# Performance work log

Measured on AMD Instinct MI355X. Metric: run time of the kernel, lower is better.

Reference implementation:

```python
import jax, jax.numpy as jnp
import numpy as np

N_NODES = 50000
N_EDGES = 800000
D_N = 64      # node feature dim
D_E = 64      # edge feature dim
HID = 128     # MLP hidden dim
D_OUT = 64    # edge/node MLP output dim


def _mlp_params(key, d_in, d_hid, d_out):
    k1, k2 = jax.random.split(key)
    s1 = 1.0 / np.sqrt(d_in)
    s2 = 1.0 / np.sqrt(d_hid)
    return (
        jax.random.uniform(k1, (d_in, d_hid), jnp.float32, -s1, s1),
        jnp.zeros((d_hid,), jnp.float32),
        jax.random.uniform(k2, (d_hid, d_out), jnp.float32, -s2, s2),
        jnp.zeros((d_out,), jnp.float32),
    )


def setup_inputs() -> dict:
    key = jax.random.key(0)
    ks = jax.random.split(key, 7)
    nf = jax.random.normal(ks[0], (N_NODES, D_N), jnp.float32)
    ef = jax.random.normal(ks[1], (N_EDGES, D_E), jnp.float32)
    src = jax.random.randint(ks[2], (N_EDGES,), 0, N_NODES, jnp.int64)
    dst = jax.random.randint(ks[3], (N_EDGES,), 0, N_NODES, jnp.int64)
    We1, be1, We2, be2 = _mlp_params(ks[4], 2 * D_N + D_E, HID, D_OUT)
    Wa1, ba1, Wa2, ba2 = _mlp_params(ks[5], 2 * D_N + D_E, HID, D_OUT)
    Wn1, bn1, Wn2, bn2 = _mlp_params(ks[6], D_OUT + D_N, HID, D_OUT)
    return dict(nf=nf, ef=ef, src=src, dst=dst,
                We1=We1, be1=be1, We2=We2, be2=be2,
                Wa1=Wa1, ba1=ba1, Wa2=Wa2, ba2=ba2,
                Wn1=Wn1, bn1=bn1, Wn2=Wn2, bn2=bn2)


def _mlp(x, W1, b1, W2, b2):
    return jax.nn.relu(x @ W1 + b1) @ W2 + b2


def reference(nf, ef, src, dst,
              We1, be1, We2, be2,
              Wa1, ba1, Wa2, ba2,
              Wn1, bn1, Wn2, bn2):
    # edge update: gather src/dst node feats, concat with edge feats  [E, 2*D_N + D_E]
    x_e = jnp.concatenate([nf[src], nf[dst], ef], axis=-1)
    e_out = _mlp(x_e, We1, be1, We2, be2)                 # [E, D_OUT]
    gate = jax.nn.sigmoid(_mlp(x_e, Wa1, ba1, Wa2, ba2))  # [E, D_OUT]
    updated_ef = gate * e_out                              # message m == updated edge feat
    # scatter-sum messages into destination nodes
    agg_m = jax.ops.segment_sum(updated_ef, dst, num_segments=N_NODES)  # [N, D_OUT]
    # node update
    x_n = jnp.concatenate([agg_m, nf], axis=-1)            # [N, D_OUT + D_N]
    updated_nf = _mlp(x_n, Wn1, bn1, Wn2, bn2)             # [N, D_OUT]
    return updated_nf, updated_ef
```

## Files before the change

### kernel.cpp

```cpp
#include <hip/hip_runtime.h>

#define NN 50000
#define NE 800000
#define NB 196

typedef float f32x4 __attribute__((ext_vector_type(4)));
typedef short s16x8 __attribute__((ext_vector_type(8)));
typedef unsigned short u16;

__device__ __forceinline__ u16 f2bf(float f) {
  union { float f; unsigned u; } v; v.f = f;
  unsigned r = v.u + 0x7FFFu + ((v.u >> 16) & 1u);
  return (u16)(r >> 16);
}

__device__ __forceinline__ void st_bf4(u16* p, f32x4 v) {
  ushort4 pv;
  pv.x = f2bf(v.x); pv.y = f2bf(v.y); pv.z = f2bf(v.z); pv.w = f2bf(v.w);
  *(ushort4*)p = pv;
}

__device__ __forceinline__ void pack_one(const float* __restrict__ W, int N,
                                         u16* __restrict__ out, int t) {
  int j = t & 7, lane = (t >> 3) & 63, f = t >> 9;
  int NT = N >> 4;
  int nt = f % NT, ks = f / NT;
  int row = ks * 32 + ((lane >> 4) << 3) + j;
  int col = nt * 16 + (lane & 15);
  out[t] = f2bf(W[row * N + col]);
}

__global__ void pack_kernel(const float* __restrict__ We1, const float* __restrict__ We2,
                            const float* __restrict__ Wa1, const float* __restrict__ Wa2,
                            const float* __restrict__ Wn1, const float* __restrict__ Wn2,
                            u16* __restrict__ out) {
  int t = blockIdx.x * 256 + threadIdx.x;
  if (t < 24576)      pack_one(We1, 128, out,          t);
  else if (t < 32768) pack_one(We2, 64,  out + 24576,  t - 24576);
  else if (t < 57344) pack_one(Wa1, 128, out + 32768,  t - 32768);
  else if (t < 65536) pack_one(Wa2, 64,  out + 57344,  t - 57344);
  else if (t < 81920) pack_one(Wn1, 128, out + 65536,  t - 65536);
  else if (t < 90112) pack_one(Wn2, 64,  out + 81920,  t - 81920);
}


__global__ void count_kernel(const int* __restrict__ dst, int* __restrict__ cnt) {
  int e = blockIdx.x * 256 + threadIdx.x;
  if (e < NE) atomicAdd(cnt + dst[e], 1);
}

__global__ __launch_bounds__(256)
void scan1_kernel(const int* __restrict__ cnt, int* __restrict__ part,
                  int* __restrict__ bsum) {
  int b = blockIdx.x, t = threadIdx.x;
  int i = b * 256 + t;
  int v = (i < NN) ? cnt[i] : 0;
  int lane = t & 63, wv = t >> 6;
  int s = v;
  #pragma unroll
  for (int d = 1; d < 64; d <<= 1) {
    int u = __shfl_up(s, d, 64);
    if (lane >= d) s += u;
  }
  __shared__ int ws[4];
  if (lane == 63) ws[wv] = s;
  __syncthreads();
  int add = 0;
  #pragma unroll
  for (int k = 0; k < 3; ++k) if (k < wv) add += ws[k];
  s += add;
  if (i < NN) part[i] = s - v;
  if (t == 255) bsum[b] = s;
}

__global__ __launch_bounds__(256)
void scan2_kernel(const int* __restrict__ bsum, int* __restrict__ bbase,
                  int* __restrict__ off) {
  int t = threadIdx.x;
  int v = (t < NB) ? bsum[t] : 0;
  int lane = t & 63, wv = t >> 6;
  int s = v;
  #pragma unroll
  for (int d = 1; d < 64; d <<= 1) {
    int u = __shfl_up(s, d, 64);
    if (lane >= d) s += u;
  }
  __shared__ int ws[4];
  if (lane == 63) ws[wv] = s;
  __syncthreads();
  int add = 0;
  #pragma unroll
  for (int k = 0; k < 3; ++k) if (k < wv) add += ws[k];
  s += add;
  if (t < NB) bbase[t] = s - v;
  if (t == NB - 1) off[NN] = s;
}

__global__ __launch_bounds__(256)
void scan3_kernel(const int* __restrict__ part, const int* __restrict__ bbase,
                  int* __restrict__ off, int* __restrict__ cursor) {
  int b = blockIdx.x, t = threadIdx.x;
  int i = b * 256 + t;
  if (i < NN) {
    int o = part[i] + bbase[b];
    off[i] = o;
    cursor[i] = o;
  }
}

__global__ void fill_kernel(const int* __restrict__ src, const int* __restrict__ dst,
                            int* __restrict__ cursor, int4* __restrict__ tup) {
  int e = blockIdx.x * 256 + threadIdx.x;
  if (e < NE) {
    int d = dst[e];
    int slot = atomicAdd(cursor + d, 1);
    int4 t4; t4.x = src[e]; t4.y = d; t4.z = e; t4.w = 0;
    tup[slot] = t4;
  }
}


__device__ __forceinline__ void edge_mlps(
    u16* xe , u16* hs , int lane,
    const u16* __restrict__ W1e, const float* __restrict__ b1e, const u16* __restrict__ W2e,
    const u16* __restrict__ W1a, const float* __restrict__ b1a, const u16* __restrict__ W2a,
    f32x4 eo[4], f32x4 go[4]) {
  const int m = lane & 15, q = lane >> 4;
  s16x8 a1[6];
  #pragma unroll
  for (int k = 0; k < 6; ++k)
    a1[k] = *(const s16x8*)(xe + m * 200 + k * 32 + q * 8);

  f32x4 acc[8];
  #pragma unroll
  for (int i = 0; i < 8; ++i) { acc[i][0] = 0.f; acc[i][1] = 0.f; acc[i][2] = 0.f; acc[i][3] = 0.f; }
  #pragma unroll
  for (int nt = 0; nt < 8; ++nt)
    #pragma unroll
    for (int k = 0; k < 6; ++k) {
      s16x8 b = *(const s16x8*)(W1e + ((size_t)(k * 8 + nt) * 64 + lane) * 8);
      acc[nt] = __builtin_amdgcn_mfma_f32_16x16x32_bf16(a1[k], b, acc[nt], 0, 0, 0);
    }
  #pragma unroll
  for (int nt = 0; nt < 8; ++nt) {
    float bv = b1e[nt * 16 + m];
    #pragma unroll
    for (int r = 0; r < 4; ++r) {
      float h = acc[nt][r] + bv;
      h = h > 0.f ? h : 0.f;
      hs[(q * 4 + r) * 136 + nt * 16 + m] = f2bf(h);
    }
  }
  __syncthreads();

  s16x8 a2[4];
  #pragma unroll
  for (int k = 0; k < 4; ++k)
    a2[k] = *(const s16x8*)(hs + m * 136 + k * 32 + q * 8);
  #pragma unroll
  for (int i = 0; i < 4; ++i) { eo[i][0] = 0.f; eo[i][1] = 0.f; eo[i][2] = 0.f; eo[i][3] = 0.f; }
  #pragma unroll
  for (int nt = 0; nt < 4; ++nt)
    #pragma unroll
    for (int k = 0; k < 4; ++k) {
      s16x8 b = *(const s16x8*)(W2e + ((size_t)(k * 4 + nt) * 64 + lane) * 8);
      eo[nt] = __builtin_amdgcn_mfma_f32_16x16x32_bf16(a2[k], b, eo[nt], 0, 0, 0);
    }

  f32x4 accg[8];
  #pragma unroll
  for (int i = 0; i < 8; ++i) { accg[i][0] = 0.f; accg[i][1] = 0.f; accg[i][2] = 0.f; accg[i][3] = 0.f; }
  #pragma unroll
  for (int nt = 0; nt < 8; ++nt)
    #pragma unroll
    for (int k = 0; k < 6; ++k) {
      s16x8 b = *(const s16x8*)(W1a + ((size_t)(k * 8 + nt) * 64 + lane) * 8);
      accg[nt] = __builtin_amdgcn_mfma_f32_16x16x32_bf16(a1[k], b, accg[nt], 0, 0, 0);
    }
  __syncthreads();
  #pragma unroll
  for (int nt = 0; nt < 8; ++nt) {
    float bv = b1a[nt * 16 + m];
    #pragma unroll
    for (int r = 0; r < 4; ++r) {
      float h = accg[nt][r] + bv;
      h = h > 0.f ? h : 0.f;
      hs[(q * 4 + r) * 136 + nt * 16 + m] = f2bf(h);
    }
  }
  __syncthreads();

  s16x8 a2g[4];
  #pragma unroll
  for (int k = 0; k < 4; ++k)
    a2g[k] = *(const s16x8*)(hs + m * 136 + k * 32 + q * 8);
  #pragma unroll
  for (int i = 0; i < 4; ++i) { go[i][0] = 0.f; go[i][1] = 0.f; go[i][2] = 0.f; go[i][3] = 0.f; }
  #pragma unroll
  for (int nt = 0; nt < 4; ++nt)
    #pragma unroll
    for (int k = 0; k < 4; ++k) {
      s16x8 b = *(const s16x8*)(W2a + ((size_t)(k * 4 + nt) * 64 + lane) * 8);
      go[nt] = __builtin_amdgcn_mfma_f32_16x16x32_bf16(a2g[k], b, go[nt], 0, 0, 0);
    }
}

__device__ __forceinline__ void node_mlp(
    u16* xn , u16* hn , int lane,
    const u16* __restrict__ W1n, const float* __restrict__ b1n, const u16* __restrict__ W2n,
    f32x4 o[4]) {
  const int m = lane & 15, q = lane >> 4;
  s16x8 a1[4];
  #pragma unroll
  for (int k = 0; k < 4; ++k)
    a1[k] = *(const s16x8*)(xn + m * 136 + k * 32 + q * 8);
  f32x4 acc[8];
  #pragma unroll
  for (int i = 0; i < 8; ++i) { acc[i][0] = 0.f; acc[i][1] = 0.f; acc[i][2] = 0.f; acc[i][3] = 0.f; }
  #pragma unroll
  for (int nt = 0; nt < 8; ++nt)
    #pragma unroll
    for (int k = 0; k < 4; ++k) {
      s16x8 b = *(const s16x8*)(W1n + ((size_t)(k * 8 + nt) * 64 + lane) * 8);
      acc[nt] = __builtin_amdgcn_mfma_f32_16x16x32_bf16(a1[k], b, acc[nt], 0, 0, 0);
    }
  #pragma unroll
  for (int nt = 0; nt < 8; ++nt) {
    float bv = b1n[nt * 16 + m];
    #pragma unroll
    for (int r = 0; r < 4; ++r) {
      float h = acc[nt][r] + bv;
      h = h > 0.f ? h : 0.f;
      hn[(q * 4 + r) * 136 + nt * 16 + m] = f2bf(h);
    }
  }
  __syncthreads();
  s16x8 a2[4];
  #pragma unroll
  for (int k = 0; k < 4; ++k)
    a2[k] = *(const s16x8*)(hn + m * 136 + k * 32 + q * 8);
  #pragma unroll
  for (int i = 0; i < 4; ++i) { o[i][0] = 0.f; o[i][1] = 0.f; o[i][2] = 0.f; o[i][3] = 0.f; }
  #pragma unroll
  for (int nt = 0; nt < 4; ++nt)
    #pragma unroll
    for (int k = 0; k < 4; ++k) {
      s16x8 b = *(const s16x8*)(W2n + ((size_t)(k * 4 + nt) * 64 + lane) * 8);
      o[nt] = __builtin_amdgcn_mfma_f32_16x16x32_bf16(a2[k], b, o[nt], 0, 0, 0);
    }
}


__global__ __launch_bounds__(256, 3)
void edge_sorted(const float* __restrict__ nf, const float* __restrict__ ef,
                 const int4* __restrict__ tup,
                 const u16* __restrict__ W1e, const float* __restrict__ b1e,
                 const u16* __restrict__ W2e, const float* __restrict__ b2e,
                 const u16* __restrict__ W1a, const float* __restrict__ b1a,
                 const u16* __restrict__ W2a, const float* __restrict__ b2a,
                 float* __restrict__ out_ef, float* __restrict__ msg) {
  __shared__ u16 xe[4][16 * 200];
  __shared__ u16 hs[4][16 * 136];
  __shared__ int se[4][16];
  const int w = threadIdx.x >> 6, lane = threadIdx.x & 63;
  const int e0 = blockIdx.x * 64 + w * 16;
  const int er = lane >> 4, c4 = (lane & 15) * 4;

  #pragma unroll
  for (int g = 0; g < 4; ++g) {
    int el = g * 4 + er;
    int slot = e0 + el;
    int4 t4 = tup[slot];
    if (c4 == 0) se[w][el] = t4.z;
    f32x4 fs = *(const f32x4*)(nf + (size_t)t4.x * 64 + c4);
    f32x4 fd = *(const f32x4*)(nf + (size_t)t4.y * 64 + c4);
    f32x4 fe = *(const f32x4*)(ef + (size_t)t4.z * 64 + c4);
    u16* row = &xe[w][el * 200];
    st_bf4(row + c4, fs);
    st_bf4(row + 64 + c4, fd);
    st_bf4(row + 128 + c4, fe);
  }
  __syncthreads();

  f32x4 eo[4], go[4];
  edge_mlps(xe[w], hs[w], lane, W1e, b1e, W2e, W1a, b1a, W2a, eo, go);

  const int m = lane & 15, q = lane >> 4;
  #pragma unroll
  for (int nt = 0; nt < 4; ++nt) {
    int col = nt * 16 + m;
    float be2v = b2e[col], ba2v = b2a[col];
    #pragma unroll
    for (int r = 0; r < 4; ++r) {
      int rowi = q * 4 + r;
      float ev = eo[nt][r] + be2v;
      float gv = go[nt][r] + ba2v;
      float gs = 1.f / (1.f + __expf(-gv));
      float val = gs * ev;
      out_ef[(size_t)se[w][rowi] * 64 + col] = val;
      msg[(size_t)(e0 + rowi) * 64 + col] = val;
    }
  }
}


__global__ __launch_bounds__(256, 3)
void edge_atomic(const float* __restrict__ nf, const float* __restrict__ ef,
                 const int* __restrict__ src, const int* __restrict__ dst,
                 const u16* __restrict__ W1e, const float* __restrict__ b1e,
                 const u16* __restrict__ W2e, const float* __restrict__ b2e,
                 const u16* __restrict__ W1a, const float* __restrict__ b1a,
                 const u16* __restrict__ W2a, const float* __restrict__ b2a,
                 float* __restrict__ out_ef, float* __restrict__ agg) {
  __shared__ u16 xe[4][16 * 200];
  __shared__ u16 hs[4][16 * 136];
  __shared__ int sdst[4][16];
  const int w = threadIdx.x >> 6, lane = threadIdx.x & 63;
  const int e0 = blockIdx.x * 64 + w * 16;
  const int er = lane >> 4, c4 = (lane & 15) * 4;

  #pragma unroll
  for (int g = 0; g < 4; ++g) {
    int el = g * 4 + er;
    int e = e0 + el;
    int s = src[e], d = dst[e];
    if (c4 == 0) sdst[w][el] = d;
    f32x4 fs = *(const f32x4*)(nf + (size_t)s * 64 + c4);
    f32x4 fd = *(const f32x4*)(nf + (size_t)d * 64 + c4);
    f32x4 fe = *(const f32x4*)(ef + (size_t)e * 64 + c4);
    u16* row = &xe[w][el * 200];
    st_bf4(row + c4, fs);
    st_bf4(row + 64 + c4, fd);
    st_bf4(row + 128 + c4, fe);
  }
  __syncthreads();

  f32x4 eo[4], go[4];
  edge_mlps(xe[w], hs[w], lane, W1e, b1e, W2e, W1a, b1a, W2a, eo, go);

  const int m = lane & 15, q = lane >> 4;
  #pragma unroll
  for (int nt = 0; nt < 4; ++nt) {
    int col = nt * 16 + m;
    float be2v = b2e[col], ba2v = b2a[col];
    #pragma unroll
    for (int r = 0; r < 4; ++r) {
      int rowi = q * 4 + r;
      float ev = eo[nt][r] + be2v;
      float gv = go[nt][r] + ba2v;
      float gs = 1.f / (1.f + __expf(-gv));
      float val = gs * ev;
      out_ef[(size_t)(e0 + rowi) * 64 + col] = val;
      atomicAdd(agg + (size_t)sdst[w][rowi] * 64 + col, val);
    }
  }
}


__global__ __launch_bounds__(256, 4)
void node_sorted(const float* __restrict__ nf, const float* __restrict__ msg,
                 const int* __restrict__ off,
                 const u16* __restrict__ W1n, const float* __restrict__ b1n,
                 const u16* __restrict__ W2n, const float* __restrict__ b2n,
                 float* __restrict__ out_nf) {
  __shared__ u16 xn[4][16 * 136];
  __shared__ u16 hn[4][16 * 136];
  const int w = threadIdx.x >> 6, lane = threadIdx.x & 63;
  const int n0 = blockIdx.x * 64 + w * 16;
  const int er = lane >> 4, c4 = (lane & 15) * 4;

  #pragma unroll
  for (int g = 0; g < 4; ++g) {
    int nl = g * 4 + er;
    int n = n0 + nl; if (n >= NN) n = NN - 1;
    f32x4 fn4 = *(const f32x4*)(nf + (size_t)n * 64 + c4);
    int beg = off[n], end = off[n + 1];
    f32x4 s0, s1, s2, s3;
    s0[0]=0.f;s0[1]=0.f;s0[2]=0.f;s0[3]=0.f; s1=s0; s2=s0; s3=s0;
    int i = beg;
    for (; i + 4 <= end; i += 4) {
      f32x4 m0 = *(const f32x4*)(msg + (size_t)(i    ) * 64 + c4);
      f32x4 m1 = *(const f32x4*)(msg + (size_t)(i + 1) * 64 + c4);
      f32x4 m2 = *(const f32x4*)(msg + (size_t)(i + 2) * 64 + c4);
      f32x4 m3 = *(const f32x4*)(msg + (size_t)(i + 3) * 64 + c4);
      s0 += m0; s1 += m1; s2 += m2; s3 += m3;
    }
    for (; i < end; ++i)
      s0 += *(const f32x4*)(msg + (size_t)i * 64 + c4);
    f32x4 s = (s0 + s1) + (s2 + s3);
    u16* row = &xn[w][nl * 136];
    st_bf4(row + c4, s);
    st_bf4(row + 64 + c4, fn4);
  }
  __syncthreads();

  f32x4 o[4];
  node_mlp(xn[w], hn[w], lane, W1n, b1n, W2n, o);

  const int m = lane & 15, q = lane >> 4;
  #pragma unroll
  for (int nt = 0; nt < 4; ++nt) {
    int col = nt * 16 + m;
    float bv = b2n[col];
    #pragma unroll
    for (int r = 0; r < 4; ++r) {
      int n = n0 + q * 4 + r;
      if (n < NN) out_nf[(size_t)n * 64 + col] = o[nt][r] + bv;
    }
  }
}


__global__ __launch_bounds__(256, 4)
void node_direct(const float* __restrict__ nf, const float* __restrict__ agg,
                 const u16* __restrict__ W1n, const float* __restrict__ b1n,
                 const u16* __restrict__ W2n, const float* __restrict__ b2n,
                 float* __restrict__ out_nf) {
  __shared__ u16 xn[4][16 * 136];
  __shared__ u16 hn[4][16 * 136];
  const int w = threadIdx.x >> 6, lane = threadIdx.x & 63;
  const int n0 = blockIdx.x * 64 + w * 16;
  const int er = lane >> 4, c4 = (lane & 15) * 4;

  #pragma unroll
  for (int g = 0; g < 4; ++g) {
    int nl = g * 4 + er;
    int n = n0 + nl; if (n >= NN) n = NN - 1;
    f32x4 fa = *(const f32x4*)(agg + (size_t)n * 64 + c4);
    f32x4 fn4 = *(const f32x4*)(nf + (size_t)n * 64 + c4);
    u16* row = &xn[w][nl * 136];
    st_bf4(row + c4, fa);
    st_bf4(row + 64 + c4, fn4);
  }
  __syncthreads();

  f32x4 o[4];
  node_mlp(xn[w], hn[w], lane, W1n, b1n, W2n, o);

  const int m = lane & 15, q = lane >> 4;
  #pragma unroll
  for (int nt = 0; nt < 4; ++nt) {
    int col = nt * 16 + m;
    float bv = b2n[col];
    #pragma unroll
    for (int r = 0; r < 4; ++r) {
      int n = n0 + q * 4 + r;
      if (n < NN) out_nf[(size_t)n * 64 + col] = o[nt][r] + bv;
    }
  }
}

extern "C" void kernel_launch(void* const* d_in, const int* in_sizes, int n_in,
                              void* d_out, int out_size, void* d_ws, size_t ws_size,
                              hipStream_t stream) {
  const float* nf  = (const float*)d_in[0];
  const float* ef  = (const float*)d_in[1];
  const int*   src = (const int*)d_in[2];
  const int*   dst = (const int*)d_in[3];
  const float* We1 = (const float*)d_in[4];
  const float* be1 = (const float*)d_in[5];
  const float* We2 = (const float*)d_in[6];
  const float* be2 = (const float*)d_in[7];
  const float* Wa1 = (const float*)d_in[8];
  const float* ba1 = (const float*)d_in[9];
  const float* Wa2 = (const float*)d_in[10];
  const float* ba2 = (const float*)d_in[11];
  const float* Wn1 = (const float*)d_in[12];
  const float* bn1 = (const float*)d_in[13];
  const float* Wn2 = (const float*)d_in[14];
  const float* bn2 = (const float*)d_in[15];
  float* out = (float*)d_out;
  float* out_ef = out + (size_t)NN * 64;

  char* ws = (char*)d_ws;
  u16* pk = (u16*)ws;

  const size_t CNT_OFF  = 180224;
  const size_t PART_OFF = 380224;
  const size_t OFF_OFF  = 580224;
  const size_t CUR_OFF  = 780240;
  const size_t BSUM_OFF = 980240;
  const size_t BBAS_OFF = 981024;
  const size_t TUP_OFF  = 981824;
  const size_t MSG_OFF  = 13781824;
  const size_t NEED     = MSG_OFF + (size_t)NE * 64 * 4;

  pack_kernel<<<352, 256, 0, stream>>>(We1, We2, Wa1, Wa2, Wn1, Wn2, pk);

  if (ws_size >= NEED) {
    int*  cnt    = (int*)(ws + CNT_OFF);
    int*  part   = (int*)(ws + PART_OFF);
    int*  off    = (int*)(ws + OFF_OFF);
    int*  cursor = (int*)(ws + CUR_OFF);
    int*  bsum   = (int*)(ws + BSUM_OFF);
    int*  bbase  = (int*)(ws + BBAS_OFF);
    int4* tup    = (int4*)(ws + TUP_OFF);
    float* msg   = (float*)(ws + MSG_OFF);

    hipMemsetAsync(cnt, 0, (size_t)NN * sizeof(int), stream);
    count_kernel<<<(NE + 255) / 256, 256, 0, stream>>>(dst, cnt);
    scan1_kernel<<<NB, 256, 0, stream>>>(cnt, part, bsum);
    scan2_kernel<<<1, 256, 0, stream>>>(bsum, bbase, off);
    scan3_kernel<<<NB, 256, 0, stream>>>(part, bbase, off, cursor);
    fill_kernel<<<(NE + 255) / 256, 256, 0, stream>>>(src, dst, cursor, tup);
    edge_sorted<<<NE / 64, 256, 0, stream>>>(nf, ef, tup,
        pk, be1, pk + 24576, be2, pk + 32768, ba1, pk + 57344, ba2,
        out_ef, msg);
    node_sorted<<<(NN + 63) / 64, 256, 0, stream>>>(nf, msg, off,
        pk + 65536, bn1, pk + 81920, bn2, out);
  } else {
    float* agg = (float*)(ws + CNT_OFF);
    hipMemsetAsync(agg, 0, (size_t)NN * 64 * sizeof(float), stream);
    edge_atomic<<<NE / 64, 256, 0, stream>>>(nf, ef, src, dst,
        pk, be1, pk + 24576, be2, pk + 32768, ba1, pk + 57344, ba2,
        out_ef, agg);
    node_direct<<<(NN + 63) / 64, 256, 0, stream>>>(nf, agg,
        pk + 65536, bn1, pk + 81920, bn2, out);
  }
}
```

Baseline: 805.3 us.

## Replace sorted message buffer with segmented atomic aggregation and XCD-aware block remap

The edge kernel no longer writes a full per-edge message buffer for a later segmented reduction. It now pre-reduces consecutive same-destination rows within each 16-edge tile, using wave shuffles when the whole tile shares one destination, and atomically adds the partial sums into a zeroed node aggregate that node_direct consumes. This removes about 200 MB of message writes and reads plus the offset array, at the cost of float atomics to global memory and a memset. Block indices are also remapped so contiguous sorted edge chunks land on the same XCD, which should improve L2 locality for the atomics.

```diff
diff --git a/kernel.cpp b/kernel.cpp
--- a/kernel.cpp
+++ b/kernel.cpp
@@ -74,8 +74,7 @@
 }
 
 __global__ __launch_bounds__(256)
-void scan2_kernel(const int* __restrict__ bsum, int* __restrict__ bbase,
-                  int* __restrict__ off) {
+void scan2_kernel(const int* __restrict__ bsum, int* __restrict__ bbase) {
   int t = threadIdx.x;
   int v = (t < NB) ? bsum[t] : 0;
   int lane = t & 63, wv = t >> 6;
@@ -93,19 +92,14 @@
   for (int k = 0; k < 3; ++k) if (k < wv) add += ws[k];
   s += add;
   if (t < NB) bbase[t] = s - v;
-  if (t == NB - 1) off[NN] = s;
 }
 
 __global__ __launch_bounds__(256)
 void scan3_kernel(const int* __restrict__ part, const int* __restrict__ bbase,
-                  int* __restrict__ off, int* __restrict__ cursor) {
+                  int* __restrict__ cursor) {
   int b = blockIdx.x, t = threadIdx.x;
   int i = b * 256 + t;
-  if (i < NN) {
-    int o = part[i] + bbase[b];
-    off[i] = o;
-    cursor[i] = o;
-  }
+  if (i < NN) cursor[i] = part[i] + bbase[b];
 }
 
 __global__ void fill_kernel(const int* __restrict__ src, const int* __restrict__ dst,
@@ -258,12 +252,17 @@
                  const u16* __restrict__ W2e, const float* __restrict__ b2e,
                  const u16* __restrict__ W1a, const float* __restrict__ b1a,
                  const u16* __restrict__ W2a, const float* __restrict__ b2a,
-                 float* __restrict__ out_ef, float* __restrict__ msg) {
+                 float* __restrict__ out_ef, float* __restrict__ agg) {
   __shared__ u16 xe[4][16 * 200];
   __shared__ u16 hs[4][16 * 136];
   __shared__ int se[4][16];
+  __shared__ int sdst[4][16];
   const int w = threadIdx.x >> 6, lane = threadIdx.x & 63;
-  const int e0 = blockIdx.x * 64 + w * 16;
+  const int nwg = gridDim.x;
+  const int qq = nwg >> 3, rr = nwg & 7;
+  const int xcd = blockIdx.x & 7, idx = blockIdx.x >> 3;
+  const int bid = (xcd < rr ? xcd * (qq + 1) : rr * (qq + 1) + (xcd - rr) * qq) + idx;
+  const int e0 = bid * 64 + w * 16;
   const int er = lane >> 4, c4 = (lane & 15) * 4;
 
   #pragma unroll
@@ -271,7 +270,7 @@
     int el = g * 4 + er;
     int slot = e0 + el;
     int4 t4 = tup[slot];
-    if (c4 == 0) se[w][el] = t4.z;
+    if (c4 == 0) { se[w][el] = t4.z; sdst[w][el] = t4.y; }
     f32x4 fs = *(const f32x4*)(nf + (size_t)t4.x * 64 + c4);
     f32x4 fd = *(const f32x4*)(nf + (size_t)t4.y * 64 + c4);
     f32x4 fe = *(const f32x4*)(ef + (size_t)t4.z * 64 + c4);
@@ -286,10 +285,13 @@
   edge_mlps(xe[w], hs[w], lane, W1e, b1e, W2e, W1a, b1a, W2a, eo, go);
 
   const int m = lane & 15, q = lane >> 4;
+  const int d0 = sdst[w][0], d15 = sdst[w][15];
+  const bool uni = (d0 == d15);
   #pragma unroll
   for (int nt = 0; nt < 4; ++nt) {
     int col = nt * 16 + m;
     float be2v = b2e[col], ba2v = b2a[col];
+    float vals[4];
     #pragma unroll
     for (int r = 0; r < 4; ++r) {
       int rowi = q * 4 + r;
@@ -298,7 +300,24 @@
       float gs = 1.f / (1.f + __expf(-gv));
       float val = gs * ev;
       out_ef[(size_t)se[w][rowi] * 64 + col] = val;
-      msg[(size_t)(e0 + rowi) * 64 + col] = val;
+      vals[r] = val;
+    }
+    if (uni) {
+      float s = (vals[0] + vals[1]) + (vals[2] + vals[3]);
+      s += __shfl_xor(s, 16, 64);
+      s += __shfl_xor(s, 32, 64);
+      if (q == 0) atomicAdd(agg + (size_t)d0 * 64 + col, s);
+    } else {
+      float run = 0.f;
+      #pragma unroll
+      for (int r = 0; r < 4; ++r) {
+        int rowi = q * 4 + r;
+        run += vals[r];
+        if (r == 3 || sdst[w][rowi] != sdst[w][rowi + 1]) {
+          atomicAdd(agg + (size_t)sdst[w][rowi] * 64 + col, run);
+          run = 0.f;
+        }
+      }
     }
   }
 }
@@ -352,60 +371,6 @@
       float val = gs * ev;
       out_ef[(size_t)(e0 + rowi) * 64 + col] = val;
       atomicAdd(agg + (size_t)sdst[w][rowi] * 64 + col, val);
-    }
-  }
-}
-
-
-__global__ __launch_bounds__(256, 4)
-void node_sorted(const float* __restrict__ nf, const float* __restrict__ msg,
-                 const int* __restrict__ off,
-                 const u16* __restrict__ W1n, const float* __restrict__ b1n,
-                 const u16* __restrict__ W2n, const float* __restrict__ b2n,
-                 float* __restrict__ out_nf) {
-  __shared__ u16 xn[4][16 * 136];
-  __shared__ u16 hn[4][16 * 136];
-  const int w = threadIdx.x >> 6, lane = threadIdx.x & 63;
-  const int n0 = blockIdx.x * 64 + w * 16;
-  const int er = lane >> 4, c4 = (lane & 15) * 4;
-
-  #pragma unroll
-  for (int g = 0; g < 4; ++g) {
-    int nl = g * 4 + er;
-    int n = n0 + nl; if (n >= NN) n = NN - 1;
-    f32x4 fn4 = *(const f32x4*)(nf + (size_t)n * 64 + c4);
-    int beg = off[n], end = off[n + 1];
-    f32x4 s0, s1, s2, s3;
-    s0[0]=0.f;s0[1]=0.f;s0[2]=0.f;s0[3]=0.f; s1=s0; s2=s0; s3=s0;
-    int i = beg;
-    for (; i + 4 <= end; i += 4) {
-      f32x4 m0 = *(const f32x4*)(msg + (size_t)(i    ) * 64 + c4);
-      f32x4 m1 = *(const f32x4*)(msg + (size_t)(i + 1) * 64 + c4);
-      f32x4 m2 = *(const f32x4*)(msg + (size_t)(i + 2) * 64 + c4);
-      f32x4 m3 = *(const f32x4*)(msg + (size_t)(i + 3) * 64 + c4);
-      s0 += m0; s1 += m1; s2 += m2; s3 += m3;
-    }
-    for (; i < end; ++i)
-      s0 += *(const f32x4*)(msg + (size_t)i * 64 + c4);
-    f32x4 s = (s0 + s1) + (s2 + s3);
-    u16* row = &xn[w][nl * 136];
-    st_bf4(row + c4, s);
-    st_bf4(row + 64 + c4, fn4);
-  }
-  __syncthreads();
-
-  f32x4 o[4];
-  node_mlp(xn[w], hn[w], lane, W1n, b1n, W2n, o);
-
-  const int m = lane & 15, q = lane >> 4;
-  #pragma unroll
-  for (int nt = 0; nt < 4; ++nt) {
-    int col = nt * 16 + m;
-    float bv = b2n[col];
-    #pragma unroll
-    for (int r = 0; r < 4; ++r) {
-      int n = n0 + q * 4 + r;
-      if (n < NN) out_nf[(size_t)n * 64 + col] = o[nt][r] + bv;
     }
   }
 }
@@ -477,36 +442,35 @@
 
   const size_t CNT_OFF  = 180224;
   const size_t PART_OFF = 380224;
-  const size_t OFF_OFF  = 580224;
-  const size_t CUR_OFF  = 780240;
-  const size_t BSUM_OFF = 980240;
-  const size_t BBAS_OFF = 981024;
-  const size_t TUP_OFF  = 981824;
-  const size_t MSG_OFF  = 13781824;
-  const size_t NEED     = MSG_OFF + (size_t)NE * 64 * 4;
+  const size_t CUR_OFF  = 580224;
+  const size_t BSUM_OFF = 780224;
+  const size_t BBAS_OFF = 781008;
+  const size_t TUP_OFF  = 781808;
+  const size_t AGG_OFF  = 13581808;
+  const size_t NEED     = AGG_OFF + (size_t)NN * 64 * 4;
 
   pack_kernel<<<352, 256, 0, stream>>>(We1, We2, Wa1, Wa2, Wn1, Wn2, pk);
 
   if (ws_size >= NEED) {
     int*  cnt    = (int*)(ws + CNT_OFF);
     int*  part   = (int*)(ws + PART_OFF);
-    int*  off    = (int*)(ws + OFF_OFF);
     int*  cursor = (int*)(ws + CUR_OFF);
     int*  bsum   = (int*)(ws + BSUM_OFF);
     int*  bbase  = (int*)(ws + BBAS_OFF);
     int4* tup    = (int4*)(ws + TUP_OFF);
-    float* msg   = (float*)(ws + MSG_OFF);
+    float* agg   = (float*)(ws + AGG_OFF);
 
     hipMemsetAsync(cnt, 0, (size_t)NN * sizeof(int), stream);
+    hipMemsetAsync(agg, 0, (size_t)NN * 64 * sizeof(float), stream);
     count_kernel<<<(NE + 255) / 256, 256, 0, stream>>>(dst, cnt);
     scan1_kernel<<<NB, 256, 0, stream>>>(cnt, part, bsum);
-    scan2_kernel<<<1, 256, 0, stream>>>(bsum, bbase, off);
-    scan3_kernel<<<NB, 256, 0, stream>>>(part, bbase, off, cursor);
+    scan2_kernel<<<1, 256, 0, stream>>>(bsum, bbase);
+    scan3_kernel<<<NB, 256, 0, stream>>>(part, bbase, cursor);
     fill_kernel<<<(NE + 255) / 256, 256, 0, stream>>>(src, dst, cursor, tup);
     edge_sorted<<<NE / 64, 256, 0, stream>>>(nf, ef, tup,
         pk, be1, pk + 24576, be2, pk + 32768, ba1, pk + 57344, ba2,
-        out_ef, msg);
-    node_sorted<<<(NN + 63) / 64, 256, 0, stream>>>(nf, msg, off,
+        out_ef, agg);
+    node_direct<<<(NN + 63) / 64, 256, 0, stream>>>(nf, agg,
         pk + 65536, bn1, pk + 81920, bn2, out);
   } else {
     float* agg = (float*)(ws + CNT_OFF);
```

Result: no change. 811.4 us (+0.8%).
